# Performance work log

Hardware: AMD Instinct MI355X
Metric: run time of the kernel (lower is better)

Reference implementation:

```python
import jax, jax.numpy as jnp
import numpy as np

D = 1024
H = 16
HD = D // H  # 64


def setup_inputs() -> dict:
    key = jax.random.key(0)
    ks = jax.random.split(key, 12)
    B, S = 2, 2048
    inp = {
        "input_query": jax.random.normal(ks[0], (B, S, D), jnp.float32),
        "input_key": jax.random.normal(ks[1], (B, S, D), jnp.float32),
        "input_value": jax.random.normal(ks[2], (B, S, D), jnp.float32),
        "mask": jnp.ones((S, S), dtype=bool),  # ignored, as in original
        # per-head Q/K/V linears, stacked over heads: [H, D, HD]
        "Wq": jax.random.normal(ks[3], (H, D, HD), jnp.float32) / np.sqrt(D),
        "bq": jax.random.normal(ks[4], (H, HD), jnp.float32) * 0.01,
        "Wk": jax.random.normal(ks[5], (H, D, HD), jnp.float32) / np.sqrt(D),
        "bk": jax.random.normal(ks[6], (H, HD), jnp.float32) * 0.01,
        "Wv": jax.random.normal(ks[7], (H, D, HD), jnp.float32) / np.sqrt(D),
        "bv": jax.random.normal(ks[8], (H, HD), jnp.float32) * 0.01,
        "Wo": jax.random.normal(ks[9], (D, D), jnp.float32) / np.sqrt(D),
        "bo": jax.random.normal(ks[10], (D,), jnp.float32) * 0.01,
    }
    return inp


def reference(input_query, input_key, input_value, mask, Wq, bq, Wk, bk, Wv, bv, Wo, bo):
    B, S, _ = input_query.shape
    # batched per-head projections: [B,S,D] x [H,D,HD] -> [B,H,S,HD]
    q = jnp.einsum("bsd,hdk->bhsk", input_query, Wq) + bq[None, :, None, :]
    k = jnp.einsum("bsd,hdk->bhsk", input_key, Wk) + bk[None, :, None, :]
    v = jnp.einsum("bsd,hdk->bhsk", input_value, Wv) + bv[None, :, None, :]
    scale = 1.0 / np.sqrt(HD)
    scores = jnp.einsum("bhqk,bhsk->bhqs", q, k) * scale  # [B,H,S,S]
    causal = jnp.tril(jnp.ones((S, S), dtype=bool))
    scores = jnp.where(causal[None, None], scores, jnp.finfo(scores.dtype).min)
    p = jax.nn.softmax(scores, axis=-1)
    out = jnp.einsum("bhqs,bhsk->bhqk", p, v)  # [B,H,S,HD]
    # concat heads (matches torch.cat over head outputs on last dim)
    out = out.transpose(0, 2, 1, 3).reshape(B, S, D)
    return out @ Wo + bo
```

## Files before the change

kernel.cpp:

```cpp
#include <hip/hip_runtime.h>
#include <hip/hip_bf16.h>

typedef __bf16 bf16;
typedef bf16 bf16x8 __attribute__((ext_vector_type(8)));
typedef bf16 bf16x4 __attribute__((ext_vector_type(4)));
typedef float f32x4 __attribute__((ext_vector_type(4)));

#define B_  2
#define S_  2048
#define D_  1024
#define H_  16
#define HD_ 64
#define M_  4096
#define K_  1024
#define N_  1024

#if __has_builtin(__builtin_amdgcn_exp2f)
#define EXP2F(x) __builtin_amdgcn_exp2f(x)
#else
#define EXP2F(x) exp2f(x)
#endif

__device__ __forceinline__ void gld16(const bf16* g, bf16* l) {
    __builtin_amdgcn_global_load_lds(
        (const __attribute__((address_space(1))) unsigned int*)(g),
        (__attribute__((address_space(3))) unsigned int*)(l), 16, 0, 0);
}

__global__ void pack_x(const float* __restrict__ xq, const float* __restrict__ xk,
                       const float* __restrict__ xv, bf16* __restrict__ out) {
    int t = blockIdx.y;
    const float* src = (t == 0) ? xq : (t == 1) ? xk : xv;
    bf16* dst = out + (size_t)t * M_ * K_;
    int idx = (blockIdx.x * 256 + threadIdx.x) * 4;
    float4 v = *(const float4*)&src[idx];
    bf16x4 o = { (bf16)v.x, (bf16)v.y, (bf16)v.z, (bf16)v.w };
    *(bf16x4*)&dst[idx] = o;
}

__global__ void pack_w(const float* __restrict__ wq, const float* __restrict__ wk,
                       const float* __restrict__ wv, const float* __restrict__ wo,
                       bf16* __restrict__ out) {
    int t = blockIdx.y;
    bf16* dst = out + (size_t)t * N_ * K_;
    int o = blockIdx.x * 256 + threadIdx.x;
    int n = o >> 10, k = o & 1023;
    if (t == 3) {
        dst[o] = (bf16)wo[k * D_ + n];
    } else {
        const float* src = (t == 0) ? wq : (t == 1) ? wk : wv;
        dst[o] = (bf16)src[(n >> 6) * (D_ * HD_) + k * HD_ + (n & 63)];
    }
}

__global__ __launch_bounds__(256) void gemm_qkv(
        const bf16* __restrict__ X, const bf16* __restrict__ Wt,
        const float* __restrict__ bq, const float* __restrict__ bk,
        const float* __restrict__ bv, bf16* __restrict__ QKV) {
    __shared__ __align__(16) bf16 As[2][128 * 32];
    __shared__ __align__(16) bf16 Bs[2][128 * 32];
    int t = blockIdx.z;
    const bf16* A = X + (size_t)t * M_ * K_;
    const bf16* W = Wt + (size_t)t * N_ * K_;
    const float* bias = (t == 0) ? bq : (t == 1) ? bk : bv;
    int m0 = blockIdx.x * 128, n0 = blockIdx.y * 128;
    int tid = threadIdx.x;
    int w = tid >> 6, l = tid & 63, lr = l & 15, lg = l >> 4;
    int wr = (w >> 1) * 64, wc = (w & 1) * 64;
    int srow = l >> 2;
    int sscol = ((l & 3) ^ ((srow >> 1) & 3)) * 8;
    int aoff[4], boff[4];
    #pragma unroll
    for (int i = 0; i < 4; i++) {
        int ra = wr + i * 16 + lr, rb = wc + i * 16 + lr;
        aoff[i] = ra * 64 + ((lg ^ ((ra >> 1) & 3)) * 16);
        boff[i] = rb * 64 + ((lg ^ ((rb >> 1) & 3)) * 16);
    }
    f32x4 acc[4][4] = {};
    #pragma unroll
    for (int c = 0; c < 2; c++) {
        int chunk = w * 2 + c;
        gld16(&A[(size_t)(m0 + chunk * 16 + srow) * K_ + sscol], &As[0][chunk * 512]);
        gld16(&W[(size_t)(n0 + chunk * 16 + srow) * K_ + sscol], &Bs[0][chunk * 512]);
    }
    __syncthreads();

    auto do_step = [&](int cb) {
        bf16x8 af[4], bfr[4];
        #pragma unroll
        for (int mi = 0; mi < 4; mi++) af[mi] = *(const bf16x8*)((const char*)As[cb] + aoff[mi]);
        #pragma unroll
        for (int ni = 0; ni < 4; ni++) bfr[ni] = *(const bf16x8*)((const char*)Bs[cb] + boff[ni]);
        #pragma unroll
        for (int mi = 0; mi < 4; mi++)
            #pragma unroll
            for (int ni = 0; ni < 4; ni++)
                acc[mi][ni] = __builtin_amdgcn_mfma_f32_16x16x32_bf16(af[mi], bfr[ni], acc[mi][ni], 0, 0, 0);
    };

    int cur = 0;
    for (int k0 = 0; k0 < K_ - 32; k0 += 32) {
        int nxt = cur ^ 1;
        #pragma unroll
        for (int c = 0; c < 2; c++) {
            int chunk = w * 2 + c;
            gld16(&A[(size_t)(m0 + chunk * 16 + srow) * K_ + k0 + 32 + sscol], &As[nxt][chunk * 512]);
            gld16(&W[(size_t)(n0 + chunk * 16 + srow) * K_ + k0 + 32 + sscol], &Bs[nxt][chunk * 512]);
        }
        do_step(cur);
        __syncthreads();
        cur = nxt;
    }
    do_step(cur);

    float qscale = (t == 0) ? 0.125f * 1.4426950408889634f : 1.0f;
    #pragma unroll
    for (int mi = 0; mi < 4; mi++)
        #pragma unroll
        for (int ni = 0; ni < 4; ni++)
            #pragma unroll
            for (int i = 0; i < 4; i++) {
                int m = m0 + wr + mi * 16 + lg * 4 + i;
                int n = n0 + wc + ni * 16 + lr;
                float v = (acc[mi][ni][i] + bias[n]) * qscale;
                int b = m >> 11, s = m & 2047, h = n >> 6, hd = n & 63;
                QKV[((((size_t)t * B_ + b) * H_ + h) * S_ + s) * HD_ + hd] = (bf16)v;
            }
}

__global__ __launch_bounds__(256) void gemm_out(
        const bf16* __restrict__ A, const bf16* __restrict__ Wt,
        const float* __restrict__ bo, float* __restrict__ out) {
    __shared__ __align__(16) bf16 As[2][128 * 32];
    __shared__ __align__(16) bf16 Bs[2][128 * 32];
    int m0 = blockIdx.x * 128, n0 = blockIdx.y * 128;
    int tid = threadIdx.x;
    int w = tid >> 6, l = tid & 63, lr = l & 15, lg = l >> 4;
    int wr = (w >> 1) * 64, wc = (w & 1) * 64;
    int srow = l >> 2;
    int sscol = ((l & 3) ^ ((srow >> 1) & 3)) * 8;
    int aoff[4], boff[4];
    #pragma unroll
    for (int i = 0; i < 4; i++) {
        int ra = wr + i * 16 + lr, rb = wc + i * 16 + lr;
        aoff[i] = ra * 64 + ((lg ^ ((ra >> 1) & 3)) * 16);
        boff[i] = rb * 64 + ((lg ^ ((rb >> 1) & 3)) * 16);
    }
    f32x4 acc[4][4] = {};
    #pragma unroll
    for (int c = 0; c < 2; c++) {
        int chunk = w * 2 + c;
        gld16(&A[(size_t)(m0 + chunk * 16 + srow) * K_ + sscol], &As[0][chunk * 512]);
        gld16(&Wt[(size_t)(n0 + chunk * 16 + srow) * K_ + sscol], &Bs[0][chunk * 512]);
    }
    __syncthreads();

    auto do_step = [&](int cb) {
        bf16x8 af[4], bfr[4];
        #pragma unroll
        for (int mi = 0; mi < 4; mi++) af[mi] = *(const bf16x8*)((const char*)As[cb] + aoff[mi]);
        #pragma unroll
        for (int ni = 0; ni < 4; ni++) bfr[ni] = *(const bf16x8*)((const char*)Bs[cb] + boff[ni]);
        #pragma unroll
        for (int mi = 0; mi < 4; mi++)
            #pragma unroll
            for (int ni = 0; ni < 4; ni++)
                acc[mi][ni] = __builtin_amdgcn_mfma_f32_16x16x32_bf16(af[mi], bfr[ni], acc[mi][ni], 0, 0, 0);
    };

    int cur = 0;
    for (int k0 = 0; k0 < K_ - 32; k0 += 32) {
        int nxt = cur ^ 1;
        #pragma unroll
        for (int c = 0; c < 2; c++) {
            int chunk = w * 2 + c;
            gld16(&A[(size_t)(m0 + chunk * 16 + srow) * K_ + k0 + 32 + sscol], &As[nxt][chunk * 512]);
            gld16(&Wt[(size_t)(n0 + chunk * 16 + srow) * K_ + k0 + 32 + sscol], &Bs[nxt][chunk * 512]);
        }
        do_step(cur);
        __syncthreads();
        cur = nxt;
    }
    do_step(cur);

    #pragma unroll
    for (int mi = 0; mi < 4; mi++)
        #pragma unroll
        for (int ni = 0; ni < 4; ni++)
            #pragma unroll
            for (int i = 0; i < 4; i++) {
                int m = m0 + wr + mi * 16 + lg * 4 + i;
                int n = n0 + wc + ni * 16 + lr;
                out[(size_t)m * N_ + n] = acc[mi][ni][i] + bo[n];
            }
}

__global__ __launch_bounds__(256) void transpose_v(const bf16* __restrict__ V,
                                                   bf16* __restrict__ VT) {
    __shared__ __align__(16) bf16 Ls[64][64];
    int s0 = blockIdx.x * 64, bh = blockIdx.y;
    const bf16* src = V + (size_t)bh * S_ * HD_;
    bf16* dst = VT + (size_t)bh * HD_ * S_;
    int tid = threadIdx.x;
    #pragma unroll
    for (int c = tid; c < 512; c += 256) {
        int row = c >> 3, cg = (c & 7) * 8;
        int cgp = cg ^ (((row >> 3) & 3) << 4);
        *(bf16x8*)&Ls[row][cgp] = *(const bf16x8*)&src[(size_t)(s0 + row) * 64 + cg];
    }
    __syncthreads();
    #pragma unroll
    for (int c = tid; c < 512; c += 256) {
        int hd = c >> 3, sg = (c & 7) * 8;
        bf16x8 v;
        #pragma unroll
        for (int e = 0; e < 8; e++) {
            int row = sg + e;
            v[e] = Ls[row][hd ^ (((row >> 3) & 3) << 4)];
        }
        *(bf16x8*)&dst[(size_t)hd * S_ + s0 + sg] = v;
    }
}

__global__ __launch_bounds__(512) void attn(const bf16* __restrict__ QKV,
                                            const bf16* __restrict__ VT,
                                            bf16* __restrict__ AO) {
    __shared__ __align__(16) bf16 Ks[2][64][72];
    __shared__ __align__(16) bf16 Vts[2][64][72];
    __shared__ __align__(16) bf16 Ps[8][16][72];
    int bh = blockIdx.y;
    int qt = (bh & 16) ? blockIdx.x : (15 - blockIdx.x);
    int q0 = qt * 128;
    const bf16* Qp = QKV + (size_t)bh * S_ * HD_;
    const bf16* Kp = QKV + (size_t)(32 + bh) * S_ * HD_;
    const bf16* VTp = VT + (size_t)bh * HD_ * S_;
    int tid = threadIdx.x, w = tid >> 6, l = tid & 63, lr = l & 15, lg = l >> 4;
    int srow = tid >> 3, scg = (tid & 7) * 8;

    bf16x8 aq[2];
    #pragma unroll
    for (int ks = 0; ks < 2; ks++)
        aq[ks] = *(const bf16x8*)&Qp[(size_t)(q0 + w * 16 + lr) * 64 + ks * 32 + lg * 8];

    f32x4 o[4] = {};
    float lsum[4] = {};
    int jmax = 2 * qt + 1;

    *(bf16x8*)&Ks[0][srow][scg]  = *(const bf16x8*)&Kp[(size_t)srow * 64 + scg];
    *(bf16x8*)&Vts[0][srow][scg] = *(const bf16x8*)&VTp[(size_t)srow * S_ + scg];
    __syncthreads();

    for (int j = 0; j <= jmax; ++j) {
        int cur = j & 1;
        bool pf = (j < jmax);
        bf16x8 kreg, vreg;
        if (pf) {
            kreg = *(const bf16x8*)&Kp[(size_t)((j + 1) * 64 + srow) * 64 + scg];
            vreg = *(const bf16x8*)&VTp[(size_t)srow * S_ + (j + 1) * 64 + scg];
        }

        f32x4 sc[4] = {};
        __builtin_amdgcn_s_setprio(1);
        #pragma unroll
        for (int ks = 0; ks < 2; ks++)
            #pragma unroll
            for (int ni = 0; ni < 4; ni++) {
                bf16x8 bk_ = *(const bf16x8*)&Ks[cur][ni * 16 + lr][ks * 32 + lg * 8];
                sc[ni] = __builtin_amdgcn_mfma_f32_16x16x32_bf16(aq[ks], bk_, sc[ni], 0, 0, 0);
            }
        __builtin_amdgcn_s_setprio(0);

        bool diag = (j >= 2 * qt);
        int qrow = w * 16 + lg * 4;
        int kvb = j * 64 - q0;
        #pragma unroll
        for (int ni = 0; ni < 4; ni++)
            #pragma unroll
            for (int i = 0; i < 4; i++) {
                float s = sc[ni][i];
                if (diag && (kvb + ni * 16 + lr > qrow + i)) s = -30000.0f;
                float p = EXP2F(s);
                lsum[i] += p;
                Ps[w][lg * 4 + i][ni * 16 + lr] = (bf16)p;
            }

        __builtin_amdgcn_s_setprio(1);
        #pragma unroll
        for (int ks = 0; ks < 2; ks++) {
            bf16x8 ap = *(const bf16x8*)&Ps[w][lr][ks * 32 + lg * 8];
            #pragma unroll
            for (int nf = 0; nf < 4; nf++) {
                bf16x8 bv_ = *(const bf16x8*)&Vts[cur][nf * 16 + lr][ks * 32 + lg * 8];
                o[nf] = __builtin_amdgcn_mfma_f32_16x16x32_bf16(ap, bv_, o[nf], 0, 0, 0);
            }
        }
        __builtin_amdgcn_s_setprio(0);

        if (pf) {
            *(bf16x8*)&Ks[cur ^ 1][srow][scg]  = kreg;
            *(bf16x8*)&Vts[cur ^ 1][srow][scg] = vreg;
        }
        __syncthreads();
    }

    #pragma unroll
    for (int i = 0; i < 4; i++) {
        #pragma unroll
        for (int xm = 1; xm < 16; xm <<= 1) lsum[i] += __shfl_xor(lsum[i], xm);
    }

    int b = bh >> 4, h = bh & 15;
    #pragma unroll
    for (int i = 0; i < 4; i++) {
        float inv = 1.0f / lsum[i];
        #pragma unroll
        for (int nf = 0; nf < 4; nf++) {
            int m = b * S_ + q0 + w * 16 + lg * 4 + i;
            int d = h * 64 + nf * 16 + lr;
            AO[(size_t)m * D_ + d] = (bf16)(o[nf][i] * inv);
        }
    }
}

extern "C" void kernel_launch(void* const* d_in, const int* in_sizes, int n_in,
                              void* d_out, int out_size, void* d_ws, size_t ws_size,
                              hipStream_t stream) {
    const float* xq = (const float*)d_in[0];
    const float* xk = (const float*)d_in[1];
    const float* xv = (const float*)d_in[2];
    const float* wq = (const float*)d_in[4];
    const float* bq = (const float*)d_in[5];
    const float* wk = (const float*)d_in[6];
    const float* bk = (const float*)d_in[7];
    const float* wv = (const float*)d_in[8];
    const float* bv = (const float*)d_in[9];
    const float* wo = (const float*)d_in[10];
    const float* bo = (const float*)d_in[11];
    float* out = (float*)d_out;

    bf16* Xb  = (bf16*)d_ws;
    bf16* Wb  = Xb  + (size_t)3 * M_ * K_;
    bf16* WoT = Wb  + (size_t)3 * N_ * K_;
    bf16* QKV = WoT + (size_t)N_ * K_;
    bf16* AO  = QKV + (size_t)3 * M_ * K_;
    bf16* VT  = Xb;

    pack_x <<<dim3(M_ * K_ / 1024, 3), 256, 0, stream>>>(xq, xk, xv, Xb);
    pack_w <<<dim3(N_ * K_ / 256, 4), 256, 0, stream>>>(wq, wk, wv, wo, Wb);
    gemm_qkv<<<dim3(M_ / 128, N_ / 128, 3), 256, 0, stream>>>(Xb, Wb, bq, bk, bv, QKV);
    transpose_v<<<dim3(S_ / 64, B_ * H_), 256, 0, stream>>>(QKV + (size_t)2 * M_ * K_, VT);
    attn    <<<dim3(S_ / 128, B_ * H_), 512, 0, stream>>>(QKV, VT, AO);
    gemm_out<<<dim3(M_ / 128, N_ / 128), 256, 0, stream>>>(AO, WoT, bo, out);
}
```

Before: 149.1 us.

## Fuse fp32-to-bf16 input conversion into QKV GEMM and split diagonal masking

```diff
diff --git a/kernel.cpp b/kernel.cpp
--- a/kernel.cpp
+++ b/kernel.cpp
@@ -20,23 +20,6 @@
 #else
 #define EXP2F(x) exp2f(x)
 #endif
-
-__device__ __forceinline__ void gld16(const bf16* g, bf16* l) {
-    __builtin_amdgcn_global_load_lds(
-        (const __attribute__((address_space(1))) unsigned int*)(g),
-        (__attribute__((address_space(3))) unsigned int*)(l), 16, 0, 0);
-}
-
-__global__ void pack_x(const float* __restrict__ xq, const float* __restrict__ xk,
-                       const float* __restrict__ xv, bf16* __restrict__ out) {
-    int t = blockIdx.y;
-    const float* src = (t == 0) ? xq : (t == 1) ? xk : xv;
-    bf16* dst = out + (size_t)t * M_ * K_;
-    int idx = (blockIdx.x * 256 + threadIdx.x) * 4;
-    float4 v = *(const float4*)&src[idx];
-    bf16x4 o = { (bf16)v.x, (bf16)v.y, (bf16)v.z, (bf16)v.w };
-    *(bf16x4*)&dst[idx] = o;
-}
 
 __global__ void pack_w(const float* __restrict__ wq, const float* __restrict__ wk,
                        const float* __restrict__ wv, const float* __restrict__ wo,
@@ -54,34 +37,52 @@
 }
 
 __global__ __launch_bounds__(256) void gemm_qkv(
-        const bf16* __restrict__ X, const bf16* __restrict__ Wt,
+        const float* __restrict__ xq, const float* __restrict__ xk,
+        const float* __restrict__ xv, const bf16* __restrict__ Wt,
         const float* __restrict__ bq, const float* __restrict__ bk,
         const float* __restrict__ bv, bf16* __restrict__ QKV) {
     __shared__ __align__(16) bf16 As[2][128 * 32];
     __shared__ __align__(16) bf16 Bs[2][128 * 32];
     int t = blockIdx.z;
-    const bf16* A = X + (size_t)t * M_ * K_;
+    const float* A = (t == 0) ? xq : (t == 1) ? xk : xv;
     const bf16* W = Wt + (size_t)t * N_ * K_;
     const float* bias = (t == 0) ? bq : (t == 1) ? bk : bv;
     int m0 = blockIdx.x * 128, n0 = blockIdx.y * 128;
     int tid = threadIdx.x;
     int w = tid >> 6, l = tid & 63, lr = l & 15, lg = l >> 4;
     int wr = (w >> 1) * 64, wc = (w & 1) * 64;
-    int srow = l >> 2;
-    int sscol = ((l & 3) ^ ((srow >> 1) & 3)) * 8;
+    int srow = tid >> 2, kslot = tid & 3;
+    const float* ag0 = A + (size_t)(m0 + srow) * K_ + kslot * 8;
+    const float* ag1 = A + (size_t)(m0 + 64 + srow) * K_ + kslot * 8;
+    const bf16*  bg0 = W + (size_t)(n0 + srow) * K_ + kslot * 8;
+    const bf16*  bg1 = W + (size_t)(n0 + 64 + srow) * K_ + kslot * 8;
+    int wo0 = (srow >> 4) * 1024 + kslot * 256 + (srow & 15) * 16;
+    int wo1 = ((64 + srow) >> 4) * 1024 + kslot * 256 + (srow & 15) * 16;
     int aoff[4], boff[4];
     #pragma unroll
     for (int i = 0; i < 4; i++) {
-        int ra = wr + i * 16 + lr, rb = wc + i * 16 + lr;
-        aoff[i] = ra * 64 + ((lg ^ ((ra >> 1) & 3)) * 16);
-        boff[i] = rb * 64 + ((lg ^ ((rb >> 1) & 3)) * 16);
+        aoff[i] = ((wr >> 4) + i) * 1024 + lg * 256 + lr * 16;
+        boff[i] = ((wc >> 4) + i) * 1024 + lg * 256 + lr * 16;
     }
     f32x4 acc[4][4] = {};
-    #pragma unroll
-    for (int c = 0; c < 2; c++) {
-        int chunk = w * 2 + c;
-        gld16(&A[(size_t)(m0 + chunk * 16 + srow) * K_ + sscol], &As[0][chunk * 512]);
-        gld16(&W[(size_t)(n0 + chunk * 16 + srow) * K_ + sscol], &Bs[0][chunk * 512]);
+
+    auto cvt8 = [](float4 a, float4 b) {
+        bf16x8 v = { (bf16)a.x, (bf16)a.y, (bf16)a.z, (bf16)a.w,
+                     (bf16)b.x, (bf16)b.y, (bf16)b.z, (bf16)b.w };
+        return v;
+    };
+
+    {
+        float4 a00 = *(const float4*)(ag0);
+        float4 a01 = *(const float4*)(ag0 + 4);
+        float4 a10 = *(const float4*)(ag1);
+        float4 a11 = *(const float4*)(ag1 + 4);
+        bf16x8 b0 = *(const bf16x8*)(bg0);
+        bf16x8 b1 = *(const bf16x8*)(bg1);
+        *(bf16x8*)((char*)As[0] + wo0) = cvt8(a00, a01);
+        *(bf16x8*)((char*)As[0] + wo1) = cvt8(a10, a11);
+        *(bf16x8*)((char*)Bs[0] + wo0) = b0;
+        *(bf16x8*)((char*)Bs[0] + wo1) = b1;
     }
     __syncthreads();
 
@@ -101,13 +102,17 @@
     int cur = 0;
     for (int k0 = 0; k0 < K_ - 32; k0 += 32) {
         int nxt = cur ^ 1;
-        #pragma unroll
-        for (int c = 0; c < 2; c++) {
-            int chunk = w * 2 + c;
-            gld16(&A[(size_t)(m0 + chunk * 16 + srow) * K_ + k0 + 32 + sscol], &As[nxt][chunk * 512]);
-            gld16(&W[(size_t)(n0 + chunk * 16 + srow) * K_ + k0 + 32 + sscol], &Bs[nxt][chunk * 512]);
-        }
+        float4 a00 = *(const float4*)(ag0 + k0 + 32);
+        float4 a01 = *(const float4*)(ag0 + k0 + 36);
+        float4 a10 = *(const float4*)(ag1 + k0 + 32);
+        float4 a11 = *(const float4*)(ag1 + k0 + 36);
+        bf16x8 b0 = *(const bf16x8*)(bg0 + k0 + 32);
+        bf16x8 b1 = *(const bf16x8*)(bg1 + k0 + 32);
         do_step(cur);
+        *(bf16x8*)((char*)As[nxt] + wo0) = cvt8(a00, a01);
+        *(bf16x8*)((char*)As[nxt] + wo1) = cvt8(a10, a11);
+        *(bf16x8*)((char*)Bs[nxt] + wo0) = b0;
+        *(bf16x8*)((char*)Bs[nxt] + wo1) = b1;
         __syncthreads();
         cur = nxt;
     }
@@ -137,21 +142,29 @@
     int tid = threadIdx.x;
     int w = tid >> 6, l = tid & 63, lr = l & 15, lg = l >> 4;
     int wr = (w >> 1) * 64, wc = (w & 1) * 64;
-    int srow = l >> 2;
-    int sscol = ((l & 3) ^ ((srow >> 1) & 3)) * 8;
+    int srow = tid >> 2, kslot = tid & 3;
+    const bf16* ag0 = A + (size_t)(m0 + srow) * K_ + kslot * 8;
+    const bf16* ag1 = A + (size_t)(m0 + 64 + srow) * K_ + kslot * 8;
+    const bf16* bg0 = Wt + (size_t)(n0 + srow) * K_ + kslot * 8;
+    const bf16* bg1 = Wt + (size_t)(n0 + 64 + srow) * K_ + kslot * 8;
+    int wo0 = (srow >> 4) * 1024 + kslot * 256 + (srow & 15) * 16;
+    int wo1 = ((64 + srow) >> 4) * 1024 + kslot * 256 + (srow & 15) * 16;
     int aoff[4], boff[4];
     #pragma unroll
     for (int i = 0; i < 4; i++) {
-        int ra = wr + i * 16 + lr, rb = wc + i * 16 + lr;
-        aoff[i] = ra * 64 + ((lg ^ ((ra >> 1) & 3)) * 16);
-        boff[i] = rb * 64 + ((lg ^ ((rb >> 1) & 3)) * 16);
+        aoff[i] = ((wr >> 4) + i) * 1024 + lg * 256 + lr * 16;
+        boff[i] = ((wc >> 4) + i) * 1024 + lg * 256 + lr * 16;
     }
     f32x4 acc[4][4] = {};
-    #pragma unroll
-    for (int c = 0; c < 2; c++) {
-        int chunk = w * 2 + c;
-        gld16(&A[(size_t)(m0 + chunk * 16 + srow) * K_ + sscol], &As[0][chunk * 512]);
-        gld16(&Wt[(size_t)(n0 + chunk * 16 + srow) * K_ + sscol], &Bs[0][chunk * 512]);
+    {
+        bf16x8 a0 = *(const bf16x8*)(ag0);
+        bf16x8 a1 = *(const bf16x8*)(ag1);
+        bf16x8 b0 = *(const bf16x8*)(bg0);
+        bf16x8 b1 = *(const bf16x8*)(bg1);
+        *(bf16x8*)((char*)As[0] + wo0) = a0;
+        *(bf16x8*)((char*)As[0] + wo1) = a1;
+        *(bf16x8*)((char*)Bs[0] + wo0) = b0;
+        *(bf16x8*)((char*)Bs[0] + wo1) = b1;
     }
     __syncthreads();
 
@@ -171,13 +184,15 @@
     int cur = 0;
     for (int k0 = 0; k0 < K_ - 32; k0 += 32) {
         int nxt = cur ^ 1;
-        #pragma unroll
-        for (int c = 0; c < 2; c++) {
-            int chunk = w * 2 + c;
-            gld16(&A[(size_t)(m0 + chunk * 16 + srow) * K_ + k0 + 32 + sscol], &As[nxt][chunk * 512]);
-            gld16(&Wt[(size_t)(n0 + chunk * 16 + srow) * K_ + k0 + 32 + sscol], &Bs[nxt][chunk * 512]);
-        }
+        bf16x8 a0 = *(const bf16x8*)(ag0 + k0 + 32);
+        bf16x8 a1 = *(const bf16x8*)(ag1 + k0 + 32);
+        bf16x8 b0 = *(const bf16x8*)(bg0 + k0 + 32);
+        bf16x8 b1 = *(const bf16x8*)(bg1 + k0 + 32);
         do_step(cur);
+        *(bf16x8*)((char*)As[nxt] + wo0) = a0;
+        *(bf16x8*)((char*)As[nxt] + wo1) = a1;
+        *(bf16x8*)((char*)Bs[nxt] + wo0) = b0;
+        *(bf16x8*)((char*)Bs[nxt] + wo1) = b1;
         __syncthreads();
         cur = nxt;
     }
@@ -270,19 +285,29 @@
             }
         __builtin_amdgcn_s_setprio(0);
 
-        bool diag = (j >= 2 * qt);
         int qrow = w * 16 + lg * 4;
         int kvb = j * 64 - q0;
-        #pragma unroll
-        for (int ni = 0; ni < 4; ni++)
-            #pragma unroll
-            for (int i = 0; i < 4; i++) {
-                float s = sc[ni][i];
-                if (diag && (kvb + ni * 16 + lr > qrow + i)) s = -30000.0f;
-                float p = EXP2F(s);
-                lsum[i] += p;
-                Ps[w][lg * 4 + i][ni * 16 + lr] = (bf16)p;
-            }
+        if (j >= 2 * qt) {
+            #pragma unroll
+            for (int ni = 0; ni < 4; ni++)
+                #pragma unroll
+                for (int i = 0; i < 4; i++) {
+                    float s = sc[ni][i];
+                    if (kvb + ni * 16 + lr > qrow + i) s = -30000.0f;
+                    float p = EXP2F(s);
+                    lsum[i] += p;
+                    Ps[w][lg * 4 + i][ni * 16 + lr] = (bf16)p;
+                }
+        } else {
+            #pragma unroll
+            for (int ni = 0; ni < 4; ni++)
+                #pragma unroll
+                for (int i = 0; i < 4; i++) {
+                    float p = EXP2F(sc[ni][i]);
+                    lsum[i] += p;
+                    Ps[w][lg * 4 + i][ni * 16 + lr] = (bf16)p;
+                }
+        }
 
         __builtin_amdgcn_s_setprio(1);
         #pragma unroll
@@ -345,9 +370,8 @@
     bf16* AO  = QKV + (size_t)3 * M_ * K_;
     bf16* VT  = Xb;
 
-    pack_x <<<dim3(M_ * K_ / 1024, 3), 256, 0, stream>>>(xq, xk, xv, Xb);
     pack_w <<<dim3(N_ * K_ / 256, 4), 256, 0, stream>>>(wq, wk, wv, wo, Wb);
-    gemm_qkv<<<dim3(M_ / 128, N_ / 128, 3), 256, 0, stream>>>(Xb, Wb, bq, bk, bv, QKV);
+    gemm_qkv<<<dim3(M_ / 128, N_ / 128, 3), 256, 0, stream>>>(xq, xk, xv, Wb, bq, bk, bv, QKV);
     transpose_v<<<dim3(S_ / 64, B_ * H_), 256, 0, stream>>>(QKV + (size_t)2 * M_ * K_, VT);
     attn    <<<dim3(S_ / 128, B_ * H_), 512, 0, stream>>>(QKV, VT, AO);
     gemm_out<<<dim3(M_ / 128, N_ / 128), 256, 0, stream>>>(AO, WoT, bo, out);
```

After: 134.1 us. -10.1%, faster.
